# Kernel tuning notes

Measured on AMD Instinct MI355X. Metric: run time of the kernel, lower is better.

The kernel has to match this reference:

```python
import jax, jax.numpy as jnp
import numpy as np

N = 8192
K = 64    # k_neighbors


def setup_inputs() -> dict:
    key = jax.random.key(0)
    k1, k2 = jax.random.split(key)
    # Unique neighbor indices per row (topk of distances in the original module
    # guarantees uniqueness per row; we mimic that with argsort of random scores
    # so scatter-set semantics are well-defined/deterministic).
    scores = jax.random.uniform(k1, (N, N), dtype=jnp.float32)
    neighbor_indices = jnp.argsort(scores, axis=-1)[:, :K].astype(jnp.int32)  # [N, K]
    adjacency_values = jax.random.normal(k2, (N, K), dtype=jnp.float32)       # [N, K]
    return {"adjacency_values": adjacency_values, "neighbor_indices": neighbor_indices}


def reference(adjacency_values, neighbor_indices):
    # Vectorized equivalent of the per-row Python scatter loop:
    #   adjacency_full[i, neighbor_indices[i]] = adjacency_values[i]
    n, k = adjacency_values.shape
    rows = jnp.arange(n)[:, None]  # [N, 1] broadcast against [N, K] column indices
    adjacency_full = jnp.zeros((n, n), dtype=adjacency_values.dtype)
    return adjacency_full.at[rows, neighbor_indices].set(adjacency_values)
```

## Files before the change

kernel.cpp:

```cpp
#include <hip/hip_runtime.h>


constexpr int N_PATCH = 8192;
constexpr int K_NB = 64;
constexpr int BLOCK = 256;
constexpr int VEC_ITERS = N_PATCH / 4 / BLOCK;

__global__ __launch_bounds__(BLOCK)
void scatter_rows_kernel(const float* __restrict__ vals,
                         const int* __restrict__ idx,
                         float* __restrict__ out) {
    const int r = blockIdx.x;
    const int t = threadIdx.x;

    int c = 0;
    float v = 0.f;
    if (t < K_NB) {
        const int base = r * K_NB + t;
        c = idx[base];
        v = vals[base];
    }
    asm volatile("" : "+v"(c), "+v"(v));

    float4* outv = reinterpret_cast<float4*>(out + (size_t)r * N_PATCH);
    const float4 z = make_float4(0.f, 0.f, 0.f, 0.f);
#pragma unroll
    for (int i = 0; i < VEC_ITERS; ++i)
        outv[t + i * BLOCK] = z;

    __syncthreads();

    if (t < K_NB)
        out[(size_t)r * N_PATCH + c] = v;
}

extern "C" void kernel_launch(void* const* d_in, const int* in_sizes, int n_in,
                              void* d_out, int out_size, void* d_ws, size_t ws_size,
                              hipStream_t stream) {
    const float* vals = (const float*)d_in[0];
    const int* idx = (const int*)d_in[1];
    float* out = (float*)d_out;

    scatter_rows_kernel<<<N_PATCH, BLOCK, 0, stream>>>(vals, idx, out);
}
```

Baseline: 261.2 us.

## Split fused per-row zero+scatter into grid-stride zero kernel and separate scatter kernel

Replaces the one-block-per-row kernel, which zeroed a row, synced, then scattered, with two launches. The first is a flat grid-stride zero fill over the whole 256 MB output using 2048 blocks. The second is a flat scatter kernel with one thread per nonzero. This removes the per-block barrier and gives the zero fill a streaming write pattern, at the cost of an extra kernel launch and a second pass of scattered writes.

```diff
diff --git a/kernel.cpp b/kernel.cpp
--- a/kernel.cpp
+++ b/kernel.cpp
@@ -3,35 +3,34 @@
 
 constexpr int N_PATCH = 8192;
 constexpr int K_NB = 64;
-constexpr int BLOCK = 256;
-constexpr int VEC_ITERS = N_PATCH / 4 / BLOCK;
 
-__global__ __launch_bounds__(BLOCK)
-void scatter_rows_kernel(const float* __restrict__ vals,
-                         const int* __restrict__ idx,
-                         float* __restrict__ out) {
-    const int r = blockIdx.x;
-    const int t = threadIdx.x;
+constexpr int ZTHREADS = 256;
+constexpr int ZBLOCKS = 2048;
+constexpr size_t TOTAL_F4 = (size_t)N_PATCH * N_PATCH / 4;
+constexpr int ZITERS = (int)(TOTAL_F4 / ((size_t)ZBLOCKS * ZTHREADS));
 
-    int c = 0;
-    float v = 0.f;
-    if (t < K_NB) {
-        const int base = r * K_NB + t;
-        c = idx[base];
-        v = vals[base];
-    }
-    asm volatile("" : "+v"(c), "+v"(v));
-
-    float4* outv = reinterpret_cast<float4*>(out + (size_t)r * N_PATCH);
+__global__ __launch_bounds__(ZTHREADS)
+void zero_kernel(float4* __restrict__ out) {
+    const size_t base = (size_t)blockIdx.x * ZTHREADS + threadIdx.x;
+    constexpr size_t STRIDE = (size_t)ZBLOCKS * ZTHREADS;
     const float4 z = make_float4(0.f, 0.f, 0.f, 0.f);
 #pragma unroll
-    for (int i = 0; i < VEC_ITERS; ++i)
-        outv[t + i * BLOCK] = z;
+    for (int i = 0; i < ZITERS; ++i)
+        out[base + (size_t)i * STRIDE] = z;
+}
 
-    __syncthreads();
+constexpr int STHREADS = 256;
+constexpr int SBLOCKS = (N_PATCH * K_NB) / STHREADS;
 
-    if (t < K_NB)
-        out[(size_t)r * N_PATCH + c] = v;
+__global__ __launch_bounds__(STHREADS)
+void scatter_kernel(const float* __restrict__ vals,
+                    const int* __restrict__ idx,
+                    float* __restrict__ out) {
+    const int g = blockIdx.x * STHREADS + threadIdx.x;
+    const int row = g >> 6;
+    const int c = idx[g];
+    const float v = vals[g];
+    out[(size_t)row * N_PATCH + c] = v;
 }
 
 extern "C" void kernel_launch(void* const* d_in, const int* in_sizes, int n_in,
@@ -41,5 +40,6 @@
     const int* idx = (const int*)d_in[1];
     float* out = (float*)d_out;
 
-    scatter_rows_kernel<<<N_PATCH, BLOCK, 0, stream>>>(vals, idx, out);
+    zero_kernel<<<ZBLOCKS, ZTHREADS, 0, stream>>>(reinterpret_cast<float4*>(out));
+    scatter_kernel<<<SBLOCKS, STHREADS, 0, stream>>>(vals, idx, out);
 }
```

Result: slower. 278.8 us (+6.7%).
